# Optimization experiments

Measured on AMD Instinct MI355X. Metric: run time of the kernel, lower is better.

## Reference

```python
import jax, jax.numpy as jnp
import numpy as np

BS, NQ, NC, NT = 64, 300, 10, 30
W_CLASS, W_BBOX, W_GIOU = 2.0, 5.0, 2.0


def cxcywh_to_xyxy(b):
    c, s = b[..., :2], b[..., 2:]
    return jnp.concatenate([c - 0.5 * s, c + 0.5 * s], axis=-1)


def _area(b):
    return (b[..., 2] - b[..., 0]) * (b[..., 3] - b[..., 1])


def giou_pairwise(a, b):
    # a: [N,4] xyxy, b: [M,4] xyxy -> [N,M]
    sum_area = _area(a)[:, None] + _area(b)[None, :]
    lt = jnp.maximum(a[:, None, :2], b[None, :, :2])
    rb = jnp.minimum(a[:, None, 2:], b[None, :, 2:])
    wh = jnp.clip(rb - lt, 0.0)
    inter = wh[..., 0] * wh[..., 1]
    union = sum_area - inter
    iou = inter / union
    ltc = jnp.minimum(a[:, None, :2], b[None, :, :2])
    rbc = jnp.maximum(a[:, None, 2:], b[None, :, 2:])
    whc = jnp.clip(rbc - ltc, 0.0)
    areac = whc[..., 0] * whc[..., 1]
    return iou - (areac - union) / areac


def giou_elementwise(a, b):
    # a, b: [N,4] xyxy -> [N]
    sum_area = _area(a) + _area(b)
    lt = jnp.maximum(a[..., :2], b[..., :2])
    rb = jnp.minimum(a[..., 2:], b[..., 2:])
    wh = jnp.clip(rb - lt, 0.0)
    inter = wh[..., 0] * wh[..., 1]
    union = sum_area - inter
    iou = inter / union
    ltc = jnp.minimum(a[..., :2], b[..., :2])
    rbc = jnp.maximum(a[..., 2:], b[..., 2:])
    whc = jnp.clip(rbc - ltc, 0.0)
    areac = whc[..., 0] * whc[..., 1]
    return iou - (areac - union) / areac


def hungarian(cost):
    # Exact rectangular assignment (Kuhn-Munkres with potentials), rows n <= cols m.
    # Returns (row_ind, col_ind) of the n matched pairs, equivalent to
    # scipy.optimize.linear_sum_assignment.
    n, m = cost.shape
    u = np.zeros(n + 1)
    v = np.zeros(m + 1)
    p = np.zeros(m + 1, dtype=np.int64)    # p[j] = row matched to col j (1-based)
    way = np.zeros(m + 1, dtype=np.int64)
    for i in range(1, n + 1):
        p[0] = i
        j0 = 0
        minv = np.full(m + 1, np.inf)
        used = np.zeros(m + 1, dtype=bool)
        while True:
            used[j0] = True
            i0 = p[j0]
            cur = cost[i0 - 1] - u[i0] - v[1:]
            mask = ~used[1:]
            better = mask & (cur < minv[1:])
            minv[1:] = np.where(better, cur, minv[1:])
            way[1:] = np.where(better, j0, way[1:])
            free = np.nonzero(mask)[0]
            j1 = free[np.argmin(minv[1:][free])] + 1
            delta = minv[j1]
            u[p[used]] += delta
            v[used] -= delta
            minv[~used] -= delta
            j0 = j1
            if p[j0] == 0:
                break
        while j0 != 0:
            j1 = way[j0]
            p[j0] = p[j1]
            j0 = j1
    rows = p[1:] - 1
    cols = np.arange(m)
    sel = rows >= 0
    return rows[sel], cols[sel]


def compute_match(pred_logits, pred_boxes, labels, boxes):
    # Mirrors @torch.no_grad() match(): build cost matrix on device, assign on host.
    bs, nq, _ = pred_logits.shape
    t = boxes.shape[1]
    out_prob = jax.nn.sigmoid(pred_logits).reshape(bs * nq, -1)
    out_bbox = pred_boxes.reshape(bs * nq, 4)
    tgt_ids = labels.reshape(-1)
    tgt_bbox = boxes.reshape(-1, 4)
    cost_class = -out_prob[:, tgt_ids]                                   # [bs*nq, bs*t]
    cost_bbox = jnp.sum(jnp.abs(out_bbox[:, None, :] - tgt_bbox[None, :, :]), -1)
    cost_giou = -giou_pairwise(cxcywh_to_xyxy(out_bbox), cxcywh_to_xyxy(tgt_bbox))
    C = W_BBOX * cost_bbox + W_CLASS * cost_class + W_GIOU * cost_giou
    C = np.asarray(jax.device_get(C), dtype=np.float64).reshape(bs, nq, bs * t)
    bidx, sidx, tidx = [], [], []
    for b in range(bs):
        block = C[b, :, b * t:(b + 1) * t]          # [nq, t]
        r, c = hungarian(block.T)                   # rows = targets, cols = queries
        bidx.extend([b] * len(c))
        sidx.extend(c.tolist())
        tidx.extend(r.tolist())
    return (np.asarray(bidx, np.int64), np.asarray(sidx, np.int64),
            np.asarray(tidx, np.int64))


def compute_loss(pred_logits, pred_boxes, labels, boxes, bidx, sidx, tidx):
    bs, nq, _ = pred_logits.shape
    num = max(1, len(bidx))
    target_classes = jnp.full((bs, nq), 10, dtype=jnp.int32)
    target_classes = target_classes.at[bidx, sidx].set(
        labels[bidx, tidx].astype(jnp.int32))
    onehot = jax.nn.one_hot(target_classes, 11, dtype=pred_logits.dtype)[..., :10]
    # sigmoid focal loss, alpha=0.25, gamma=2, reduction='sum'
    x, t = pred_logits, onehot
    p = jax.nn.sigmoid(x)
    ce = jnp.maximum(x, 0.0) - x * t + jnp.log1p(jnp.exp(-jnp.abs(x)))
    p_t = p * t + (1.0 - p) * (1.0 - t)
    alpha_t = 0.25 * t + 0.75 * (1.0 - t)
    loss_ce = jnp.sum(alpha_t * ce * (1.0 - p_t) ** 2) / num
    src_boxes = pred_boxes[bidx, sidx]
    tgt_boxes = boxes[bidx, tidx]
    loss_bbox = jnp.sum(jnp.abs(src_boxes - tgt_boxes)) / num
    g = giou_elementwise(cxcywh_to_xyxy(src_boxes), cxcywh_to_xyxy(tgt_boxes))
    loss_giou = jnp.sum(1.0 - g) / num
    return loss_ce + 5.0 * loss_bbox + 2.0 * loss_giou


def setup_inputs() -> dict:
    key = jax.random.key(0)
    k0, k1, k2, k3 = jax.random.split(key, 4)
    pred_logits = jax.random.normal(k0, (BS, NQ, NC), dtype=jnp.float32)
    pred_boxes = jax.random.uniform(k1, (BS, NQ, 4), dtype=jnp.float32)
    labels = jax.random.randint(k2, (BS, NT), 0, 10, dtype=jnp.int64)
    boxes = jax.random.uniform(k3, (BS, NT, 4), dtype=jnp.float32)
    return {"pred_logits": pred_logits, "pred_boxes": pred_boxes,
            "labels": labels, "boxes": boxes}


def reference(pred_logits, pred_boxes, labels, boxes):
    bidx, sidx, tidx = compute_match(pred_logits, pred_boxes, labels, boxes)
    return compute_loss(pred_logits, pred_boxes, labels, boxes, bidx, sidx, tidx)
```

## Files before the change

kernel.cpp:

```cpp
#include <hip/hip_runtime.h>
#include <math.h>

#define NQ 300
#define NQP 301
#define NT 30
#define NC 10
#define NTH 512
#define NWAVE 8
#define INFF 3.0e38f

__device__ __forceinline__ float sigf(float x){ return 1.0f/(1.0f + __expf(-x)); }
__device__ __forceinline__ float softplusf(float x){ return fmaxf(x,0.0f) + __logf(1.0f + __expf(-fabsf(x))); }
__device__ __forceinline__ float focal0(float x){
  float pr = sigf(x);
  return 0.75f * softplusf(x) * pr * pr;
}
__device__ __forceinline__ float readlane_f(float v, int l){
  return __int_as_float(__builtin_amdgcn_readlane(__float_as_int(v), l));
}
__device__ __forceinline__ int readlane_i(int v, int l){
  return __builtin_amdgcn_readlane(v, l);
}

template<int CTRL,int RMASK>
__device__ __forceinline__ float dppmin_f(float x){
  int t = __builtin_amdgcn_update_dpp(0x7f800000, __float_as_int(x), CTRL, RMASK, 0xf, false);
  return fminf(x, __int_as_float(t));
}
template<int CTRL,int RMASK>
__device__ __forceinline__ unsigned dppmin_u(unsigned x){
  unsigned t = (unsigned)__builtin_amdgcn_update_dpp((int)0xFFFFFFFFu, (int)x, CTRL, RMASK, 0xf, false);
  return x < t ? x : t;
}
template<int CTRL,int RMASK>
__device__ __forceinline__ float dppadd_f(float x){
  int t = __builtin_amdgcn_update_dpp(0, __float_as_int(x), CTRL, RMASK, 0xf, false);
  return x + __int_as_float(t);
}
__device__ __forceinline__ void wave_argmin64(float v, unsigned idx, float &ov, int &oj){
  float x = v;
  x = dppmin_f<0x111,0xf>(x); x = dppmin_f<0x112,0xf>(x);
  x = dppmin_f<0x114,0xf>(x); x = dppmin_f<0x118,0xf>(x);
  x = dppmin_f<0x142,0xa>(x); x = dppmin_f<0x143,0xc>(x);
  float vmin = __int_as_float(__builtin_amdgcn_readlane(__float_as_int(x), 63));
  unsigned c = (v == vmin) ? idx : 0xFFFFFFFFu;
  c = dppmin_u<0x111,0xf>(c); c = dppmin_u<0x112,0xf>(c);
  c = dppmin_u<0x114,0xf>(c); c = dppmin_u<0x118,0xf>(c);
  c = dppmin_u<0x142,0xa>(c); c = dppmin_u<0x143,0xc>(c);
  oj = __builtin_amdgcn_readlane((int)c, 63);
  ov = vmin;
}
__device__ __forceinline__ float wave_sum64(float v){
  float x = v;
  x = dppadd_f<0x111,0xf>(x); x = dppadd_f<0x112,0xf>(x);
  x = dppadd_f<0x114,0xf>(x); x = dppadd_f<0x118,0xf>(x);
  x = dppadd_f<0x142,0xa>(x); x = dppadd_f<0x143,0xc>(x);
  return __int_as_float(__builtin_amdgcn_readlane(__float_as_int(x), 63));
}

__global__ __launch_bounds__(NTH) void hm_main(
    const float* __restrict__ logits,
    const float* __restrict__ pbox,
    const int*   __restrict__ labels,
    const float* __restrict__ tbox,
    float* __restrict__ out)
{
  const int bid = blockIdx.x;
  const int tid = threadIdx.x;
  const int wv = tid >> 6, ln = tid & 63;

  __shared__ float D[NT*NQ];
  __shared__ float psmT[NC*NQP];
  __shared__ float traw[NT][4], txy[NT][4], tarea[NT];
  __shared__ int   tlab[NT];
  __shared__ float uu[NT+1];
  __shared__ int   pcol[NQ];
  __shared__ int   claimA[NQ];
  __shared__ int   rargm[NT];
  __shared__ float redw[NWAVE];

  if (bid >= 64) {
    const int b = bid - 64;
    const float4* lg4 = (const float4*)(logits + (size_t)b*NQ*NC);
    float tot = 0.f;
    for (int e = tid; e < NQ*NC/4; e += NTH) {
      float4 v = lg4[e];
      tot += focal0(v.x) + focal0(v.y) + focal0(v.z) + focal0(v.w);
    }
    float wsum = wave_sum64(tot);
    if (ln == 0) redw[wv] = wsum;
    __syncthreads();
    if (tid == 0) {
      float s = 0.f;
      #pragma unroll
      for (int w = 0; w < NWAVE; ++w) s += redw[w];
      atomicAdd(out, s * (1.0f/1920.0f));
    }
    return;
  }

  const int b = bid;
  const bool v4 = ln < (NQ - 256);

  float qcx[5],qcy[5],qw[5],qh[5],qx0[5],qy0[5],qx1[5],qy1[5],qar[5];
  {
    const float4* pb4 = (const float4*)pbox + (size_t)b*NQ;
    #pragma unroll
    for (int k = 0; k < 5; ++k) {
      float4 s = (k < 4 || v4) ? pb4[ln + (k<<6)] : make_float4(0.f,0.f,0.f,0.f);
      qcx[k]=s.x; qcy[k]=s.y; qw[k]=s.z; qh[k]=s.w;
      qx0[k]=s.x-0.5f*s.z; qy0[k]=s.y-0.5f*s.w;
      qx1[k]=s.x+0.5f*s.z; qy1[k]=s.y+0.5f*s.w;
      qar[k]=(qx1[k]-qx0[k])*(qy1[k]-qy0[k]);
    }
  }
  if (tid < NT) {
    float4 s = ((const float4*)tbox)[(size_t)b*NT + tid];
    traw[tid][0]=s.x; traw[tid][1]=s.y; traw[tid][2]=s.z; traw[tid][3]=s.w;
    float x0=s.x-0.5f*s.z, y0=s.y-0.5f*s.w, x1=s.x+0.5f*s.z, y1=s.y+0.5f*s.w;
    txy[tid][0]=x0; txy[tid][1]=y0; txy[tid][2]=x1; txy[tid][3]=y1;
    tarea[tid]=(x1-x0)*(y1-y0);
    tlab[tid]=labels[b*NT + tid];
  }
  for (int j = tid; j < NQ; j += NTH) { pcol[j]=0; claimA[j]=0x7fffffff; }

  {
    const float4* lg4 = (const float4*)(logits + (size_t)b*NQ*NC);
    for (int e4 = tid; e4 < NQ*NC/4; e4 += NTH) {
      float4 v = lg4[e4];
      int e = e4 << 2;
      #pragma unroll
      for (int j = 0; j < 4; ++j) {
        float x = (j==0)?v.x:(j==1)?v.y:(j==2)?v.z:v.w;
        int ee = e + j, q = ee / NC, c = ee - q*NC;
        psmT[c*NQP + q] = sigf(x);
      }
    }
  }
  __syncthreads();

  for (int i = wv; i < NT; i += NWAVE) {
    const float t0=traw[i][0], t1=traw[i][1], t2=traw[i][2], t3=traw[i][3];
    const float x0=txy[i][0], y0=txy[i][1], x1=txy[i][2], y1=txy[i][3];
    const float ta=tarea[i];
    const float* prow = &psmT[tlab[i]*NQP];
    float bv=INFF; unsigned bj=0xFFFFFFFFu;
    #pragma unroll
    for (int k = 0; k < 5; ++k) {
      if (k < 4 || v4) {
        int q = ln + (k<<6);
        float cb = fabsf(qcx[k]-t0)+fabsf(qcy[k]-t1)+fabsf(qw[k]-t2)+fabsf(qh[k]-t3);
        float lt0=fmaxf(qx0[k],x0), lt1=fmaxf(qy0[k],y0);
        float rb0=fminf(qx1[k],x1), rb1=fminf(qy1[k],y1);
        float iw=fmaxf(rb0-lt0,0.f), ih=fmaxf(rb1-lt1,0.f);
        float inter=iw*ih;
        float uni=qar[k]+ta-inter;
        float iou=inter/uni;
        float c0=fminf(qx0[k],x0), c1=fminf(qy0[k],y0);
        float c2=fmaxf(qx1[k],x1), c3=fmaxf(qy1[k],y1);
        float cw=fmaxf(c2-c0,0.f), ch=fmaxf(c3-c1,0.f);
        float areac=cw*ch;
        float g=iou-(areac-uni)/areac;
        float dval = 5.f*cb - 2.f*prow[q] - 2.f*g;
        D[i*NQ+q] = dval;
        if (dval < bv) { bv=dval; bj=(unsigned)q; }
      }
    }
    float vmin; int jmin;
    wave_argmin64(bv, bj, vmin, jmin);
    if (ln == 0) { uu[i+1]=vmin; rargm[i]=jmin; }
  }
  __syncthreads();

  if (wv == 0) {
    const int lane = ln;
    float u_reg = (lane < NT) ? uu[lane+1] : 0.f;
    float vv0=0.f,vv1=0.f,vv2=0.f,vv3=0.f,vv4=0.f;
    int jm = (lane < NT) ? rargm[lane] : 0;
    bool winner = false;
    if (lane < NT) {
      atomicMin(&claimA[jm], lane);
      winner = (claimA[jm] == lane);
      if (winner) pcol[jm] = lane + 1;
    }
    unsigned freerows = (unsigned)__ballot(lane < NT && !winner);
    int pc0=pcol[lane], pc1=pcol[lane+64], pc2=pcol[lane+128], pc3=pcol[lane+192];
    int pc4 = v4 ? pcol[lane+256] : 0;
    int wy0=0, wy1=0, wy2=0, wy3=0, wy4=0;

    while (freerows) {
      int fr = __builtin_ctz(freerows); freerows &= (freerows - 1);
      const int it = fr + 1;
      float mn0=INFF,mn1=INFF,mn2=INFF,mn3=INFF,mn4=INFF;
      int usedm = 0;
      bool onpath = (lane == fr);
      int j0 = -1, i0 = it, j1 = 0;
      for (;;) {
        float ui0 = readlane_f(u_reg, i0-1);
        const float* Drow = &D[(i0-1)*NQ];
        float lval = INFF; unsigned lidx = 0xFFFFFFFFu;
        #define SCAN_K(K, MN, VV, WY) \
          if ((K < 4 || v4) && !((usedm>>K)&1)) { \
            float cur = Drow[lane + (K<<6)] - ui0 - VV; \
            if (cur < MN) { MN = cur; WY = j0; } \
            if (MN < lval) { lval = MN; lidx = (unsigned)(lane + (K<<6)); } \
          }
        SCAN_K(0, mn0, vv0, wy0)
        SCAN_K(1, mn1, vv1, wy1)
        SCAN_K(2, mn2, vv2, wy2)
        SCAN_K(3, mn3, vv3, wy3)
        SCAN_K(4, mn4, vv4, wy4)
        #undef SCAN_K
        float delta; int j1i;
        wave_argmin64(lval, lidx, delta, j1i);
        j1 = j1i;
        if (onpath) u_reg += delta;
        #define UPD_K(K, MN, VV) if ((usedm>>K)&1) VV -= delta; else MN -= delta;
        UPD_K(0, mn0, vv0) UPD_K(1, mn1, vv1) UPD_K(2, mn2, vv2)
        UPD_K(3, mn3, vv3) UPD_K(4, mn4, vv4)
        #undef UPD_K
        int slot = j1 >> 6, src = j1 & 63;
        int pv;
        switch (slot) { case 0: pv=pc0; break; case 1: pv=pc1; break;
                        case 2: pv=pc2; break; case 3: pv=pc3; break; default: pv=pc4; }
        int pj1 = readlane_i(pv, src);
        if (pj1 == 0) break;
        onpath = onpath || (lane == (pj1-1));
        if (lane == src) usedm |= (1 << slot);
        j0 = j1; i0 = pj1;
      }
      int j = j1;
      for (;;) {
        int slot = j >> 6, src = j & 63;
        int wval;
        switch (slot) { case 0: wval=wy0; break; case 1: wval=wy1; break;
                        case 2: wval=wy2; break; case 3: wval=wy3; break; default: wval=wy4; }
        int jp = readlane_i(wval, src);
        int rr;
        if (jp < 0) rr = it;
        else {
          int s2 = jp >> 6, l2 = jp & 63;
          int pv2;
          switch (s2) { case 0: pv2=pc0; break; case 1: pv2=pc1; break;
                        case 2: pv2=pc2; break; case 3: pv2=pc3; break; default: pv2=pc4; }
          rr = readlane_i(pv2, l2);
        }
        switch (slot) {
          case 0: if (lane==src) pc0=rr; break;
          case 1: if (lane==src) pc1=rr; break;
          case 2: if (lane==src) pc2=rr; break;
          case 3: if (lane==src) pc3=rr; break;
          default: if (lane==src) pc4=rr; break;
        }
        if (jp < 0) break;
        j = jp;
      }
    }
    pcol[lane]=pc0; pcol[lane+64]=pc1; pcol[lane+128]=pc2; pcol[lane+192]=pc3;
    if (v4) pcol[lane+256]=pc4;
  }
  __syncthreads();

  float tot = 0.f;
  if (wv < 5 && (wv < 4 || v4)) {
    int q = ln + (wv<<6);
    int row = pcol[q];
    if (row > 0) {
      int ti = row-1;
      float scx,scy,sw,sh,sx0,sy0,sx1,sy1,sar;
      switch (wv) {
        case 0: scx=qcx[0];scy=qcy[0];sw=qw[0];sh=qh[0];sx0=qx0[0];sy0=qy0[0];sx1=qx1[0];sy1=qy1[0];sar=qar[0]; break;
        case 1: scx=qcx[1];scy=qcy[1];sw=qw[1];sh=qh[1];sx0=qx0[1];sy0=qy0[1];sx1=qx1[1];sy1=qy1[1];sar=qar[1]; break;
        case 2: scx=qcx[2];scy=qcy[2];sw=qw[2];sh=qh[2];sx0=qx0[2];sy0=qy0[2];sx1=qx1[2];sy1=qy1[2];sar=qar[2]; break;
        case 3: scx=qcx[3];scy=qcy[3];sw=qw[3];sh=qh[3];sx0=qx0[3];sy0=qy0[3];sx1=qx1[3];sy1=qy1[3];sar=qar[3]; break;
        default: scx=qcx[4];scy=qcy[4];sw=qw[4];sh=qh[4];sx0=qx0[4];sy0=qy0[4];sx1=qx1[4];sy1=qy1[4];sar=qar[4]; break;
      }
      float l1 = fabsf(scx-traw[ti][0])+fabsf(scy-traw[ti][1])
               + fabsf(sw -traw[ti][2])+fabsf(sh -traw[ti][3]);
      float lt0=fmaxf(sx0,txy[ti][0]), lt1=fmaxf(sy0,txy[ti][1]);
      float rb0=fminf(sx1,txy[ti][2]), rb1=fminf(sy1,txy[ti][3]);
      float iw=fmaxf(rb0-lt0,0.f), ih=fmaxf(rb1-lt1,0.f);
      float inter=iw*ih;
      float uni=sar+tarea[ti]-inter;
      float iou=inter/uni;
      float c0=fminf(sx0,txy[ti][0]), c1=fminf(sy0,txy[ti][1]);
      float c2=fmaxf(sx1,txy[ti][2]), c3=fmaxf(sy1,txy[ti][3]);
      float cw=fmaxf(c2-c0,0.f), ch=fmaxf(c3-c1,0.f);
      float areac=cw*ch;
      float g=iou-(areac-uni)/areac;
      float x  = logits[((size_t)b*NQ+q)*NC + tlab[ti]];
      float pr = psmT[tlab[ti]*NQP + q];
      float sp = softplusf(x);
      tot += (0.25f*(sp - x)*(1.f-pr)*(1.f-pr) - 0.75f*sp*pr*pr) + 5.f*l1 + 2.f*(1.f-g);
    }
  }
  float wsum = wave_sum64(tot);
  if (ln == 0) redw[wv] = wsum;
  __syncthreads();
  if (tid == 0) {
    float s = 0.f;
    #pragma unroll
    for (int w = 0; w < NWAVE; ++w) s += redw[w];
    atomicAdd(out, s * (1.0f/1920.0f));
  }
}

extern "C" void kernel_launch(void* const* d_in, const int* in_sizes, int n_in,
                              void* d_out, int out_size, void* d_ws, size_t ws_size,
                              hipStream_t stream) {
  const float* logits = (const float*)d_in[0];
  const float* pbox   = (const float*)d_in[1];
  const int*   labels = (const int*)d_in[2];
  const float* tbox   = (const float*)d_in[3];
  hipMemsetAsync(d_out, 0, sizeof(float), stream);
  hm_main<<<dim3(128), dim3(NTH), 0, stream>>>(logits, pbox, labels, tbox, (float*)d_out);
}
```

Baseline: 24.82 us.

## Add auction-style augmenting row reduction before Hungarian shortest-path phase

Adds an augmenting row reduction phase, in the style of the Jonker-Volgenant algorithm, before the shortest-path loop. For each free row it finds the best and second-best reduced cost with a combined wave-wide DPP reduction over monotone-encoded keys, assigns the best column, updates the column potential and row dual, and re-queues any row it displaces. The phase is capped at 96 iterations. It is meant to cut the number of costly Dijkstra-style augmentations, at the price of extra passes over each row and some branching.

```diff
diff --git a/kernel.cpp b/kernel.cpp
--- a/kernel.cpp
+++ b/kernel.cpp
@@ -20,6 +20,13 @@
 }
 __device__ __forceinline__ int readlane_i(int v, int l){
   return __builtin_amdgcn_readlane(v, l);
+}
+__device__ __forceinline__ unsigned monof(float x){
+  unsigned u = __float_as_uint(x);
+  return (u >> 31) ? ~u : (u | 0x80000000u);
+}
+__device__ __forceinline__ float invmonof(unsigned m){
+  return (m & 0x80000000u) ? __uint_as_float(m & 0x7fffffffu) : __uint_as_float(~m);
 }
 
 template<int CTRL,int RMASK>
@@ -56,6 +63,24 @@
   x = dppadd_f<0x114,0xf>(x); x = dppadd_f<0x118,0xf>(x);
   x = dppadd_f<0x142,0xa>(x); x = dppadd_f<0x143,0xc>(x);
   return __int_as_float(__builtin_amdgcn_readlane(__float_as_int(x), 63));
+}
+__device__ __forceinline__ void wave_min2(unsigned k1m, unsigned k1i, unsigned k2m,
+                                          unsigned &o1m, unsigned &o1i, unsigned &o2m){
+  #define LVL(CTRL,RMASK) { \
+    unsigned n1m = (unsigned)__builtin_amdgcn_update_dpp((int)0xFFFFFFFFu,(int)k1m,CTRL,RMASK,0xf,false); \
+    unsigned n1i = (unsigned)__builtin_amdgcn_update_dpp((int)0xFFFFFFFFu,(int)k1i,CTRL,RMASK,0xf,false); \
+    unsigned n2m = (unsigned)__builtin_amdgcn_update_dpp((int)0xFFFFFFFFu,(int)k2m,CTRL,RMASK,0xf,false); \
+    bool nw = (n1m < k1m) || (n1m == k1m && n1i < k1i); \
+    unsigned lose = nw ? k1m : n1m; \
+    unsigned t2 = k2m < n2m ? k2m : n2m; \
+    k2m = t2 < lose ? t2 : lose; \
+    k1m = nw ? n1m : k1m; k1i = nw ? n1i : k1i; }
+  LVL(0x111,0xf) LVL(0x112,0xf) LVL(0x114,0xf) LVL(0x118,0xf)
+  LVL(0x142,0xa) LVL(0x143,0xc)
+  #undef LVL
+  o1m = (unsigned)__builtin_amdgcn_readlane((int)k1m, 63);
+  o1i = (unsigned)__builtin_amdgcn_readlane((int)k1i, 63);
+  o2m = (unsigned)__builtin_amdgcn_readlane((int)k2m, 63);
 }
 
 __global__ __launch_bounds__(NTH) void hm_main(
@@ -187,6 +212,44 @@
     int pc0=pcol[lane], pc1=pcol[lane+64], pc2=pcol[lane+128], pc3=pcol[lane+192];
     int pc4 = v4 ? pcol[lane+256] : 0;
     int wy0=0, wy1=0, wy2=0, wy3=0, wy4=0;
+
+    int arr_it = 0;
+    while (freerows && ++arr_it <= 96) {
+      int fr = __builtin_ctz(freerows); freerows &= (freerows - 1);
+      const float* Drow = &D[fr*NQ];
+      float rv0=INFF,rv1=INFF,rv2=INFF,rv3=INFF,rv4=INFF;
+      unsigned l1m=0xFFFFFFFFu, l1i=0xFFFFFFFFu, l2m=0xFFFFFFFFu;
+      #define ARR_K(K, VV, RV) \
+        if (K < 4 || v4) { \
+          RV = Drow[lane + (K<<6)] - VV; \
+          unsigned mm = monof(RV); unsigned ii = (unsigned)(lane + (K<<6)); \
+          if (mm < l1m) { l2m = l1m; l1m = mm; l1i = ii; } \
+          else { l2m = l2m < mm ? l2m : mm; } \
+        }
+      ARR_K(0, vv0, rv0) ARR_K(1, vv1, rv1) ARR_K(2, vv2, rv2)
+      ARR_K(3, vv3, rv3) ARR_K(4, vv4, rv4)
+      #undef ARR_K
+      unsigned m1m, j1u, m2m;
+      wave_min2(l1m, l1i, l2m, m1m, j1u, m2m);
+      float m2f = invmonof(m2m);
+      int j1 = (int)j1u;
+      int slot = j1 >> 6, src = j1 & 63;
+      int pv;
+      switch (slot) { case 0: pv=pc0; break; case 1: pv=pc1; break;
+                      case 2: pv=pc2; break; case 3: pv=pc3; break; default: pv=pc4; }
+      int prevrow = readlane_i(pv, src);
+      if (lane == fr) u_reg = m2f;
+      if (lane == src) {
+        switch (slot) {
+          case 0: vv0 += (rv0 - m2f); pc0 = fr+1; break;
+          case 1: vv1 += (rv1 - m2f); pc1 = fr+1; break;
+          case 2: vv2 += (rv2 - m2f); pc2 = fr+1; break;
+          case 3: vv3 += (rv3 - m2f); pc3 = fr+1; break;
+          default: vv4 += (rv4 - m2f); pc4 = fr+1; break;
+        }
+      }
+      if (prevrow != 0) freerows |= (1u << (prevrow-1));
+    }
 
     while (freerows) {
       int fr = __builtin_ctz(freerows); freerows &= (freerows - 1);
```

Measured after the change: 26.22 us. +5.6%, slower.
